# Optimization experiments

Hardware: AMD Instinct MI355X
Metric: run time of the kernel (lower is better)

Reference implementation:

```python
import jax, jax.numpy as jnp
import numpy as np

WINDOW = 8
HEADS = 16
HIDDEN = 256
EMBED = HIDDEN * WINDOW          # 2048
HEAD_DIM = EMBED // HEADS        # 128
BATCH = 8
SEQ = 4096                       # multiple of WINDOW
GROUP = SEQ // WINDOW            # 512


def _indices():
    # index_one[i*g + j] = j*w + i  (residue-class grouping permutation)
    i = np.arange(WINDOW)
    j = np.arange(GROUP)
    index_one = (j[None, :] * WINDOW + i[:, None]).reshape(-1)
    # index_two[i*w + k] = k*g + i  (inverse-style interleave permutation)
    index_two = (np.arange(WINDOW)[None, :] * GROUP + np.arange(GROUP)[:, None]).reshape(-1)
    return jnp.asarray(index_one), jnp.asarray(index_two)


def _attention(M, Wq, Wk, Wv, fc_w, fc_b):
    # M: [N, g, E] with E = heads*head_dim
    N, L, E = M.shape
    x = M.reshape(N, L, HEADS, HEAD_DIM)
    q = jnp.einsum('nlhd,ed->nlhe', x, Wq)
    k = jnp.einsum('nlhd,ed->nlhe', x, Wk)
    v = jnp.einsum('nlhd,ed->nlhe', x, Wv)
    energy = jnp.einsum('nqhd,nkhd->nhqk', q, k)
    attn = jax.nn.softmax(energy / jnp.sqrt(jnp.float32(EMBED)), axis=-1)
    out = jnp.einsum('nhqk,nkhd->nqhd', attn, v).reshape(N, L, E)
    return out @ fc_w.T + fc_b


def setup_inputs() -> dict:
    key = jax.random.key(0)
    ks = jax.random.split(key, 6)
    s = 0.02
    return {
        'M': jax.random.normal(ks[0], (BATCH, SEQ, HIDDEN), jnp.float32),
        'Wq': jax.random.normal(ks[1], (HEAD_DIM, HEAD_DIM), jnp.float32) * s,
        'Wk': jax.random.normal(ks[2], (HEAD_DIM, HEAD_DIM), jnp.float32) * s,
        'Wv': jax.random.normal(ks[3], (HEAD_DIM, HEAD_DIM), jnp.float32) * s,
        'fc_w': jax.random.normal(ks[4], (EMBED, EMBED), jnp.float32) * s,
        'fc_b': jax.random.normal(ks[5], (EMBED,), jnp.float32) * s,
        'device': 0,
    }


def reference(M, Wq, Wk, Wv, fc_w, fc_b, device):
    del device  # unused, mirrors torch signature
    index_one, index_two = _indices()
    N, S, H = M.shape
    w, g = WINDOW, GROUP
    for b in range(w):
        idx = (index_one - b) % S
        M = M[:, idx]                                             # gather permute
        # segmentation step 1: [N, w*g, H] -> [N, g, w*H]
        M = M.reshape(N, w, g, H).transpose(0, 2, 1, 3).reshape(N, g, w * H)
        M = _attention(M, Wq, Wk, Wv, fc_w, fc_b)
        # segmentation step 2: [N, g, w*H] -> [N, w*g, H]
        M = M.reshape(N, g, w, H).transpose(0, 2, 1, 3).reshape(N, w * g, H)
        # index_two rotated once per iteration after the first -> roll by -b
        M = M[:, jnp.roll(index_two, -b)]
    return M[:, :S]
```

## Files before the change

kernel.cpp:

```cpp
#include <hip/hip_runtime.h>
#include <stdint.h>

typedef unsigned short u16;
typedef unsigned int u32;
typedef __bf16 bf16x8 __attribute__((ext_vector_type(8)));
typedef float f32x4 __attribute__((ext_vector_type(4)));
typedef float f32x16 __attribute__((ext_vector_type(16)));
typedef u16 u16x4 __attribute__((ext_vector_type(4)));
typedef u16 u16x8 __attribute__((ext_vector_type(8)));

#define MFMA16(a, b, c) __builtin_amdgcn_mfma_f32_16x16x32_bf16(a, b, c, 0, 0, 0)
#define MFMA32(a, b, c) __builtin_amdgcn_mfma_f32_32x32x16_bf16(a, b, c, 0, 0, 0)

__device__ __forceinline__ u16 f2bf(float f) {
  u32 u = __builtin_bit_cast(u32, f);
  u += 0x7FFFu + ((u >> 16) & 1u);
  return (u16)(u >> 16);
}

__device__ __forceinline__ bf16x8 ld16(const u16* p) {
  return __builtin_bit_cast(bf16x8, *(const uint4*)p);
}

__device__ __forceinline__ void gl_lds(const u16* src, u16* lds) {
  __builtin_amdgcn_global_load_lds(
      (const __attribute__((address_space(1))) u32*)src,
      (__attribute__((address_space(3))) u32*)lds, 16, 0, 0);
}

__global__ __launch_bounds__(256) void convert_weights(
    const float* __restrict__ Wq, const float* __restrict__ Wk,
    const float* __restrict__ Wv, const float* __restrict__ fcw,
    u16* __restrict__ wq_b, u16* __restrict__ wk_b, u16* __restrict__ wv_b,
    u16* __restrict__ fcw_b) {
  int bx = blockIdx.x, tid = threadIdx.x;
  if (bx < 4096) {
    int i = (bx * 256 + tid) * 4;
    float4 f = *(const float4*)&fcw[i];
    u16x4 o = {f2bf(f.x), f2bf(f.y), f2bf(f.z), f2bf(f.w)};
    *(u16x4*)&fcw_b[i] = o;
  } else {
    int i = ((bx - 4096) * 256 + tid) * 4;
    const float sc = 0.022097086912079612f;
    float4 q = *(const float4*)&Wq[i];
    u16x4 oq = {f2bf(q.x * sc), f2bf(q.y * sc), f2bf(q.z * sc), f2bf(q.w * sc)};
    *(u16x4*)&wq_b[i] = oq;
    float4 k = *(const float4*)&Wk[i];
    u16x4 ok = {f2bf(k.x), f2bf(k.y), f2bf(k.z), f2bf(k.w)};
    *(u16x4*)&wk_b[i] = ok;
    float4 v = *(const float4*)&Wv[i];
    u16x4 ov = {f2bf(v.x), f2bf(v.y), f2bf(v.z), f2bf(v.w)};
    *(u16x4*)&wv_b[i] = ov;
  }
}

__global__ __launch_bounds__(768) void qkv_kernel(
    const float* __restrict__ srcF, const u16* __restrict__ srcB, int srcf32,
    const u16* __restrict__ wq, const u16* __restrict__ wk,
    const u16* __restrict__ wvw, u16* __restrict__ Q, u16* __restrict__ K,
    u16* __restrict__ Vt, int bsh) {
  __shared__ u16 X[64 * 264];
  int jt = blockIdx.x, i0 = blockIdx.y, n = blockIdx.z;
  int tid = threadIdx.x;
#pragma unroll
  for (int it = 0; it < 3; ++it) {
    int c = tid + it * 768;
    if (c < 2048) {
      int row = c >> 5, seg = c & 31;
      int pos = (8 * (jt * 64 + row) + i0 - bsh) & 4095;
      size_t base = ((size_t)n * 4096 + pos) * 256 + seg * 8;
      if (srcf32) {
        float4 f0 = *(const float4*)&srcF[base];
        float4 f1 = *(const float4*)&srcF[base + 4];
        u16x8 v = {f2bf(f0.x), f2bf(f0.y), f2bf(f0.z), f2bf(f0.w),
                   f2bf(f1.x), f2bf(f1.y), f2bf(f1.z), f2bf(f1.w)};
        *(u16x8*)&X[row * 264 + seg * 8] = v;
      } else {
        *(u16x8*)&X[row * 264 + seg * 8] = *(const u16x8*)&srcB[base];
      }
    }
  }
  __syncthreads();
  int wvid = tid >> 6, ln = tid & 63;
  int mat = wvid >> 2, hc = wvid & 3;
  int hh = hc >> 1, cb = (hc & 1) * 64;
  int h = i0 * 2 + hh, xc = hh * 128;
  const u16* W = (mat == 0) ? wq : (mat == 1) ? wk : wvw;
  int lr = ln & 15, lg = ln >> 4;
  f32x4 acc[4][4] = {};
#pragma unroll
  for (int kt = 0; kt < 4; ++kt) {
    bf16x8 a[4], b[4];
#pragma unroll
    for (int mt = 0; mt < 4; ++mt)
      a[mt] = ld16(&X[(mt * 16 + lr) * 264 + xc + kt * 32 + lg * 8]);
#pragma unroll
    for (int nc = 0; nc < 4; ++nc)
      b[nc] = ld16(&W[(cb + nc * 16 + lr) * 128 + kt * 32 + lg * 8]);
#pragma unroll
    for (int mt = 0; mt < 4; ++mt)
#pragma unroll
      for (int nc = 0; nc < 4; ++nc)
        acc[mt][nc] = MFMA16(a[mt], b[nc], acc[mt][nc]);
  }
  size_t nh = (size_t)(n * 16 + h);
  if (mat < 2) {
    u16* dst = (mat == 0 ? Q : K) + nh * 512 * 128;
#pragma unroll
    for (int mt = 0; mt < 4; ++mt)
#pragma unroll
      for (int nc = 0; nc < 4; ++nc) {
        int col = cb + nc * 16 + lr;
        int jb = jt * 64 + mt * 16 + lg * 4;
#pragma unroll
        for (int r = 0; r < 4; ++r)
          dst[(size_t)(jb + r) * 128 + col] = f2bf(acc[mt][nc][r]);
      }
  } else {
    u16* dst = Vt + nh * 128 * 512;
#pragma unroll
    for (int mt = 0; mt < 4; ++mt)
#pragma unroll
      for (int nc = 0; nc < 4; ++nc) {
        int col = cb + nc * 16 + lr;
        int jb = jt * 64 + mt * 16 + lg * 4;
        u16x4 pk = {f2bf(acc[mt][nc][0]), f2bf(acc[mt][nc][1]),
                    f2bf(acc[mt][nc][2]), f2bf(acc[mt][nc][3])};
        *(u16x4*)&dst[(size_t)col * 512 + jb] = pk;
      }
  }
}

__global__ __launch_bounds__(256, 2) void attn_kernel(
    const u16* __restrict__ Q, const u16* __restrict__ K,
    const u16* __restrict__ Vt, u16* __restrict__ O) {
  __shared__ u16 KL[2][64 * 128];
  __shared__ u16 VL[2][128 * 64];
  int flat = blockIdx.x;
  int xcd = flat & 7, idx = flat >> 3;
  int gl = idx & 15, qt = idx >> 4;
  int g = xcd | (gl << 3);
  int h = g & 15, n = g >> 4;
  int tid = threadIdx.x, wv = tid >> 6, ln = tid & 63;
  int l31 = ln & 31, hh = ln >> 5;
  size_t nh = (size_t)(n * 16 + h);
  int q0 = qt * 128 + wv * 32;
  const u16* Qb = Q + ((size_t)nh * 512 + q0) * 128;
  const u16* Kb = K + (size_t)nh * 512 * 128;
  const u16* Vb = Vt + (size_t)nh * 128 * 512;

  bf16x8 qf[8];
#pragma unroll
  for (int kt = 0; kt < 8; ++kt)
    qf[kt] = ld16(&Qb[l31 * 128 + kt * 16 + hh * 8]);

  int l16 = ln & 15, l8 = ln & 7;
  int rK[4], cK[4], rV[4], cV[4];
#pragma unroll
  for (int i = 0; i < 4; ++i) {
    int s = wv * 4 + i;
    rK[i] = 4 * s + (ln >> 4);
    cK[i] = (l16 ^ (rK[i] & 15)) * 8;
    rV[i] = 8 * s + (ln >> 3);
    cV[i] = (l8 ^ (rV[i] & 7)) * 8;
  }

#pragma unroll
  for (int i = 0; i < 4; ++i) {
    int s = wv * 4 + i;
    gl_lds(&Kb[(size_t)rK[i] * 128 + cK[i]], &KL[0][s * 512]);
    gl_lds(&Vb[(size_t)rV[i] * 512 + 0 * 64 + cV[i]], &VL[0][s * 512]);
  }
  __syncthreads();

  f32x16 o[4] = {};
  float m = -1e30f, l = 0.f;

  for (int kv = 0; kv < 8; ++kv) {
    int cur = kv & 1;
    if (kv < 7) {
      int nxt = cur ^ 1;
      const u16* kp = Kb + (size_t)(kv + 1) * 64 * 128;
#pragma unroll
      for (int i = 0; i < 4; ++i) {
        int s = wv * 4 + i;
        gl_lds(&kp[(size_t)rK[i] * 128 + cK[i]], &KL[nxt][s * 512]);
        gl_lds(&Vb[(size_t)rV[i] * 512 + (kv + 1) * 64 + cV[i]], &VL[nxt][s * 512]);
      }
    }
    f32x16 s[2] = {};
    __builtin_amdgcn_s_setprio(1);
#pragma unroll
    for (int kb = 0; kb < 2; ++kb)
#pragma unroll
      for (int kt = 0; kt < 8; ++kt) {
        int row = kb * 32 + l31;
        int slot = (2 * kt + hh) ^ (row & 15);
        bf16x8 a = ld16(&KL[cur][row * 128 + slot * 8]);
        s[kb] = MFMA32(a, qf[kt], s[kb]);
      }
    __builtin_amdgcn_s_setprio(0);
    float mx[8];
#pragma unroll
    for (int i = 0; i < 8; ++i)
      mx[i] = fmaxf(fmaxf(s[0][2 * i], s[0][2 * i + 1]),
                    fmaxf(s[1][2 * i], s[1][2 * i + 1]));
    float pm = fmaxf(fmaxf(fmaxf(mx[0], mx[1]), fmaxf(mx[2], mx[3])),
                     fmaxf(fmaxf(mx[4], mx[5]), fmaxf(mx[6], mx[7])));
    pm = fmaxf(pm, __shfl_xor(pm, 32));
    if (!__all(pm <= m + 8.f)) {
      float nm = fmaxf(m, pm);
      float al = __expf(m - nm);
      l *= al;
      m = nm;
#pragma unroll
      for (int r = 0; r < 16; ++r) {
        int qr = (r & 3) + 8 * (r >> 2) + 4 * hh;
        float av = __shfl(al, (ln & 32) | qr, 64);
        o[0][r] *= av; o[1][r] *= av; o[2][r] *= av; o[3][r] *= av;
      }
    }
#pragma unroll
    for (int kb = 0; kb < 2; ++kb)
#pragma unroll
      for (int r = 0; r < 16; ++r) s[kb][r] = __expf(s[kb][r] - m);
    float sm[8];
#pragma unroll
    for (int i = 0; i < 8; ++i)
      sm[i] = (s[0][2 * i] + s[0][2 * i + 1]) + (s[1][2 * i] + s[1][2 * i + 1]);
    float rs = ((sm[0] + sm[1]) + (sm[2] + sm[3])) +
               ((sm[4] + sm[5]) + (sm[6] + sm[7]));
    rs += __shfl_xor(rs, 32);
    l += rs;
    bf16x8 pa[4];
#pragma unroll
    for (int ks = 0; ks < 4; ++ks) {
      const int kb = ks >> 1, r0 = 8 * (ks & 1);
      u32 wA, wB, wC, wD;
      asm("v_cvt_pk_bf16_f32 %0, %1, %2" : "=v"(wA) : "v"(s[kb][r0 + 0]), "v"(s[kb][r0 + 1]));
      asm("v_cvt_pk_bf16_f32 %0, %1, %2" : "=v"(wB) : "v"(s[kb][r0 + 2]), "v"(s[kb][r0 + 3]));
      asm("v_cvt_pk_bf16_f32 %0, %1, %2" : "=v"(wC) : "v"(s[kb][r0 + 4]), "v"(s[kb][r0 + 5]));
      asm("v_cvt_pk_bf16_f32 %0, %1, %2" : "=v"(wD) : "v"(s[kb][r0 + 6]), "v"(s[kb][r0 + 7]));
      asm("v_permlane32_swap_b32 %0, %1" : "+v"(wA), "+v"(wC));
      asm("v_permlane32_swap_b32 %0, %1" : "+v"(wB), "+v"(wD));
      uint4 ww = {wA, wB, wC, wD};
      pa[ks] = __builtin_bit_cast(bf16x8, ww);
    }
    __builtin_amdgcn_s_setprio(1);
#pragma unroll
    for (int ks = 0; ks < 4; ++ks)
#pragma unroll
      for (int nb = 0; nb < 4; ++nb) {
        int row = nb * 32 + l31;
        int slot = (2 * ks + hh) ^ (row & 7);
        bf16x8 bv = ld16(&VL[cur][row * 64 + slot * 8]);
        o[nb] = MFMA32(pa[ks], bv, o[nb]);
      }
    __builtin_amdgcn_s_setprio(0);
    if (kv < 7) __syncthreads();
  }
  float inv = 1.f / l;
#pragma unroll
  for (int r = 0; r < 16; ++r) {
    int qr = (r & 3) + 8 * (r >> 2) + 4 * hh;
    float iv = __shfl(inv, (ln & 32) | qr, 64);
    int row = q0 + qr;
    u16* dst = O + ((size_t)n * 512 + row) * 2048 + h * 128;
    dst[0 * 32 + l31] = f2bf(o[0][r] * iv);
    dst[1 * 32 + l31] = f2bf(o[1][r] * iv);
    dst[2 * 32 + l31] = f2bf(o[2][r] * iv);
    dst[3 * 32 + l31] = f2bf(o[3][r] * iv);
  }
}

__global__ __launch_bounds__(256, 2) void fc_kernel(
    const u16* __restrict__ A, const u16* __restrict__ Bw,
    const float* __restrict__ bias, float* __restrict__ doutF,
    u16* __restrict__ doutB, int last, int bsh) {
  __shared__ u16 AL[2][128 * 64];
  __shared__ u16 BL[2][128 * 64];
  int bn = blockIdx.x, bm = blockIdx.y;
  int tid = threadIdx.x, wv = tid >> 6, ln = tid & 63;
  int lr = ln & 15, lg = ln >> 4;
  int R0 = bm * 128, C0 = bn * 128;
  int wr = (wv & 1) * 64, wc = (wv >> 1) * 64;
  const u16 *gAsrc[4], *gBsrc[4];
  int srow[4];
#pragma unroll
  for (int i = 0; i < 4; ++i) {
    int r = i * 32 + wv * 8 + (ln >> 3);
    int cs = ((ln & 7) ^ (r & 7)) * 8;
    gAsrc[i] = A + (size_t)(R0 + r) * 2048 + cs;
    gBsrc[i] = Bw + (size_t)(C0 + r) * 2048 + cs;
    srow[i] = i * 32 + wv * 8;
  }
  int aoff[4][2], boff[4][2];
#pragma unroll
  for (int i = 0; i < 4; ++i) {
    int ra = wr + i * 16 + lr, rb = wc + i * 16 + lr;
#pragma unroll
    for (int kk = 0; kk < 2; ++kk) {
      aoff[i][kk] = ra * 64 + (((kk * 4 + lg) ^ (ra & 7)) * 8);
      boff[i][kk] = rb * 64 + (((kk * 4 + lg) ^ (rb & 7)) * 8);
    }
  }
  f32x4 acc[4][4] = {};
#pragma unroll
  for (int i = 0; i < 4; ++i) {
    gl_lds(gAsrc[i], &AL[0][srow[i] * 64]);
    gl_lds(gBsrc[i], &BL[0][srow[i] * 64]);
  }
  for (int t = 0; t < 32; ++t) {
    int cur = t & 1, nx = cur ^ 1;
    if (t < 31) {
      int k0 = (t + 1) * 64;
#pragma unroll
      for (int i = 0; i < 4; ++i) {
        gl_lds(gAsrc[i] + k0, &AL[nx][srow[i] * 64]);
        gl_lds(gBsrc[i] + k0, &BL[nx][srow[i] * 64]);
      }
      asm volatile("s_waitcnt vmcnt(8)" ::: "memory");
    } else {
      asm volatile("s_waitcnt vmcnt(0)" ::: "memory");
    }
    __builtin_amdgcn_s_barrier();
#pragma unroll
    for (int kk = 0; kk < 2; ++kk) {
      bf16x8 a[4], b[4];
#pragma unroll
      for (int i = 0; i < 4; ++i) a[i] = ld16(&AL[cur][aoff[i][kk]]);
#pragma unroll
      for (int i = 0; i < 4; ++i) b[i] = ld16(&BL[cur][boff[i][kk]]);
      __builtin_amdgcn_s_setprio(1);
#pragma unroll
      for (int mt = 0; mt < 4; ++mt)
#pragma unroll
        for (int nc = 0; nc < 4; ++nc)
          acc[mt][nc] = MFMA16(a[mt], b[nc], acc[mt][nc]);
      __builtin_amdgcn_s_setprio(0);
    }
    if (t < 31) __builtin_amdgcn_s_barrier();
  }
#pragma unroll
  for (int nc = 0; nc < 4; ++nc) {
    int e = C0 + wc + nc * 16 + lr;
    float bv = bias[e];
    int i = e >> 8, cc = e & 255;
#pragma unroll
    for (int mt = 0; mt < 4; ++mt)
#pragma unroll
      for (int r = 0; r < 4; ++r) {
        int row = R0 + wr + mt * 16 + lg * 4 + r;
        int nn = row >> 9, j = row & 511;
        int pos = (8 * j + i - bsh) & 4095;
        size_t di = ((size_t)nn * 4096 + pos) * 256 + cc;
        float v = acc[mt][nc][r] + bv;
        if (last) doutF[di] = v;
        else doutB[di] = f2bf(v);
      }
  }
}

extern "C" void kernel_launch(void* const* d_in, const int* in_sizes, int n_in,
                              void* d_out, int out_size, void* d_ws, size_t ws_size,
                              hipStream_t stream) {
  const float* M = (const float*)d_in[0];
  const float* Wq = (const float*)d_in[1];
  const float* Wk = (const float*)d_in[2];
  const float* Wv = (const float*)d_in[3];
  const float* fcw = (const float*)d_in[4];
  const float* fcb = (const float*)d_in[5];
  float* out = (float*)d_out;
  char* ws = (char*)d_ws;
  u16* wq_b = (u16*)(ws + (0 << 10));
  u16* wk_b = (u16*)(ws + (32 << 10));
  u16* wv_b = (u16*)(ws + (64 << 10));
  u16* fcw_b = (u16*)(ws + (128 << 10));
  u16* Qb = (u16*)(ws + ((size_t)16 << 20));
  u16* Kb = (u16*)(ws + ((size_t)32 << 20));
  u16* Vtb = (u16*)(ws + ((size_t)48 << 20));
  u16* Ab = (u16*)(ws + ((size_t)64 << 20));
  u16* Sb = (u16*)(ws + ((size_t)96 << 20));

  convert_weights<<<4112, 256, 0, stream>>>(Wq, Wk, Wv, fcw, wq_b, wk_b, wv_b, fcw_b);
  for (int b = 0; b < 8; ++b) {
    qkv_kernel<<<dim3(8, 8, 8), 768, 0, stream>>>(M, Sb, (b == 0) ? 1 : 0,
                                                  wq_b, wk_b, wv_b, Qb, Kb, Vtb, b);
    attn_kernel<<<512, 256, 0, stream>>>(Qb, Kb, Vtb, Ab);
    fc_kernel<<<dim3(16, 32), 256, 0, stream>>>(Ab, fcw_b, fcb, out, Sb,
                                                (b == 7) ? 1 : 0, b);
  }
}
```

Measured before the change: 722.6 us.

## Enlarge FC GEMM tile to 128x256 with interleaved B-loads between MFMA phases

The FC GEMM now uses 512-thread blocks computing 128x256 output tiles (256 blocks instead of 512), so each A tile is reused across twice as many columns. The K-loop is split into four MFMA phases separated by barriers, and the next B tile's global-to-LDS loads are issued in halves between phases so memory traffic overlaps with compute. The intent is to cut global load traffic and hide load latency. In exchange it adds more barriers per iteration, needs more LDS per block, and 256 blocks may not fill all CUs as well as before.

```diff
diff --git a/kernel.cpp b/kernel.cpp
--- a/kernel.cpp
+++ b/kernel.cpp
@@ -273,26 +273,35 @@
   }
 }
 
-__global__ __launch_bounds__(256, 2) void fc_kernel(
+__global__ __launch_bounds__(512, 1) void fc_kernel(
     const u16* __restrict__ A, const u16* __restrict__ Bw,
     const float* __restrict__ bias, float* __restrict__ doutF,
     u16* __restrict__ doutB, int last, int bsh) {
   __shared__ u16 AL[2][128 * 64];
-  __shared__ u16 BL[2][128 * 64];
-  int bn = blockIdx.x, bm = blockIdx.y;
+  __shared__ u16 BL[2][256 * 64];
+  int blk = blockIdx.x;
+  int bm = blk >> 3, bn = blk & 7;
   int tid = threadIdx.x, wv = tid >> 6, ln = tid & 63;
   int lr = ln & 15, lg = ln >> 4;
-  int R0 = bm * 128, C0 = bn * 128;
-  int wr = (wv & 1) * 64, wc = (wv >> 1) * 64;
-  const u16 *gAsrc[4], *gBsrc[4];
-  int srow[4];
+  int R0 = bm * 128, C0 = bn * 256;
+  int wr = (wv >> 2) * 64, wc = (wv & 3) * 64;
+  const u16* gA[2];
+  int sA[2];
+  const u16* gB[4];
+  int sB[4];
+#pragma unroll
+  for (int i = 0; i < 2; ++i) {
+    int r = wv * 16 + i * 8 + (ln >> 3);
+    int cs = ((ln & 7) ^ (r & 7)) * 8;
+    gA[i] = A + (size_t)(R0 + r) * 2048 + cs;
+    sA[i] = (wv * 16 + i * 8) * 64;
+  }
 #pragma unroll
   for (int i = 0; i < 4; ++i) {
-    int r = i * 32 + wv * 8 + (ln >> 3);
+    int r = wv * 32 + i * 8 + (ln >> 3);
     int cs = ((ln & 7) ^ (r & 7)) * 8;
-    gAsrc[i] = A + (size_t)(R0 + r) * 2048 + cs;
-    gBsrc[i] = Bw + (size_t)(C0 + r) * 2048 + cs;
-    srow[i] = i * 32 + wv * 8;
+    gB[i] = Bw + (size_t)(C0 + r) * 2048 + cs;
+    sB[i] = (wv * 32 + i * 8) * 64;
   }
   int aoff[4][2], boff[4][2];
 #pragma unroll
@@ -306,40 +315,89 @@
   }
   f32x4 acc[4][4] = {};
 #pragma unroll
-  for (int i = 0; i < 4; ++i) {
-    gl_lds(gAsrc[i], &AL[0][srow[i] * 64]);
-    gl_lds(gBsrc[i], &BL[0][srow[i] * 64]);
-  }
+  for (int i = 0; i < 2; ++i) gl_lds(gA[i], &AL[0][sA[i]]);
+#pragma unroll
+  for (int i = 0; i < 4; ++i) gl_lds(gB[i], &BL[0][sB[i]]);
+
   for (int t = 0; t < 32; ++t) {
     int cur = t & 1, nx = cur ^ 1;
+    int k0 = (t + 1) * 64;
     if (t < 31) {
-      int k0 = (t + 1) * 64;
-#pragma unroll
-      for (int i = 0; i < 4; ++i) {
-        gl_lds(gAsrc[i] + k0, &AL[nx][srow[i] * 64]);
-        gl_lds(gBsrc[i] + k0, &BL[nx][srow[i] * 64]);
-      }
-      asm volatile("s_waitcnt vmcnt(8)" ::: "memory");
+      gl_lds(gA[0] + k0, &AL[nx][sA[0]]);
+      gl_lds(gA[1] + k0, &AL[nx][sA[1]]);
+      asm volatile("s_waitcnt vmcnt(2)" ::: "memory");
     } else {
       asm volatile("s_waitcnt vmcnt(0)" ::: "memory");
     }
     __builtin_amdgcn_s_barrier();
-#pragma unroll
-    for (int kk = 0; kk < 2; ++kk) {
-      bf16x8 a[4], b[4];
-#pragma unroll
-      for (int i = 0; i < 4; ++i) a[i] = ld16(&AL[cur][aoff[i][kk]]);
-#pragma unroll
-      for (int i = 0; i < 4; ++i) b[i] = ld16(&BL[cur][boff[i][kk]]);
+    bf16x8 b0 = ld16(&BL[cur][boff[0][0]]), b1 = ld16(&BL[cur][boff[1][0]]);
+    bf16x8 b2 = ld16(&BL[cur][boff[2][0]]), b3 = ld16(&BL[cur][boff[3][0]]);
+    {
+      bf16x8 a0 = ld16(&AL[cur][aoff[0][0]]), a1 = ld16(&AL[cur][aoff[1][0]]);
       __builtin_amdgcn_s_setprio(1);
-#pragma unroll
-      for (int mt = 0; mt < 4; ++mt)
-#pragma unroll
-        for (int nc = 0; nc < 4; ++nc)
-          acc[mt][nc] = MFMA16(a[mt], b[nc], acc[mt][nc]);
+      acc[0][0] = MFMA16(a0, b0, acc[0][0]);
+      acc[0][1] = MFMA16(a0, b1, acc[0][1]);
+      acc[0][2] = MFMA16(a0, b2, acc[0][2]);
+      acc[0][3] = MFMA16(a0, b3, acc[0][3]);
+      acc[1][0] = MFMA16(a1, b0, acc[1][0]);
+      acc[1][1] = MFMA16(a1, b1, acc[1][1]);
+      acc[1][2] = MFMA16(a1, b2, acc[1][2]);
+      acc[1][3] = MFMA16(a1, b3, acc[1][3]);
       __builtin_amdgcn_s_setprio(0);
     }
-    if (t < 31) __builtin_amdgcn_s_barrier();
+    __builtin_amdgcn_s_barrier();
+    if (t < 31) {
+      gl_lds(gB[0] + k0, &BL[nx][sB[0]]);
+      gl_lds(gB[1] + k0, &BL[nx][sB[1]]);
+    }
+    {
+      bf16x8 a2 = ld16(&AL[cur][aoff[2][0]]), a3 = ld16(&AL[cur][aoff[3][0]]);
+      __builtin_amdgcn_s_setprio(1);
+      acc[2][0] = MFMA16(a2, b0, acc[2][0]);
+      acc[2][1] = MFMA16(a2, b1, acc[2][1]);
+      acc[2][2] = MFMA16(a2, b2, acc[2][2]);
+      acc[2][3] = MFMA16(a2, b3, acc[2][3]);
+      acc[3][0] = MFMA16(a3, b0, acc[3][0]);
+      acc[3][1] = MFMA16(a3, b1, acc[3][1]);
+      acc[3][2] = MFMA16(a3, b2, acc[3][2]);
+      acc[3][3] = MFMA16(a3, b3, acc[3][3]);
+      __builtin_amdgcn_s_setprio(0);
+    }
+    __builtin_amdgcn_s_barrier();
+    if (t < 31) {
+      gl_lds(gB[2] + k0, &BL[nx][sB[2]]);
+      gl_lds(gB[3] + k0, &BL[nx][sB[3]]);
+    }
+    b0 = ld16(&BL[cur][boff[0][1]]); b1 = ld16(&BL[cur][boff[1][1]]);
+    b2 = ld16(&BL[cur][boff[2][1]]); b3 = ld16(&BL[cur][boff[3][1]]);
+    {
+      bf16x8 a0 = ld16(&AL[cur][aoff[0][1]]), a1 = ld16(&AL[cur][aoff[1][1]]);
+      __builtin_amdgcn_s_setprio(1);
+      acc[0][0] = MFMA16(a0, b0, acc[0][0]);
+      acc[0][1] = MFMA16(a0, b1, acc[0][1]);
+      acc[0][2] = MFMA16(a0, b2, acc[0][2]);
+      acc[0][3] = MFMA16(a0, b3, acc[0][3]);
+      acc[1][0] = MFMA16(a1, b0, acc[1][0]);
+      acc[1][1] = MFMA16(a1, b1, acc[1][1]);
+      acc[1][2] = MFMA16(a1, b2, acc[1][2]);
+      acc[1][3] = MFMA16(a1, b3, acc[1][3]);
+      __builtin_amdgcn_s_setprio(0);
+    }
+    __builtin_amdgcn_s_barrier();
+    {
+      bf16x8 a2 = ld16(&AL[cur][aoff[2][1]]), a3 = ld16(&AL[cur][aoff[3][1]]);
+      __builtin_amdgcn_s_setprio(1);
+      acc[2][0] = MFMA16(a2, b0, acc[2][0]);
+      acc[2][1] = MFMA16(a2, b1, acc[2][1]);
+      acc[2][2] = MFMA16(a2, b2, acc[2][2]);
+      acc[2][3] = MFMA16(a2, b3, acc[2][3]);
+      acc[3][0] = MFMA16(a3, b0, acc[3][0]);
+      acc[3][1] = MFMA16(a3, b1, acc[3][1]);
+      acc[3][2] = MFMA16(a3, b2, acc[3][2]);
+      acc[3][3] = MFMA16(a3, b3, acc[3][3]);
+      __builtin_amdgcn_s_setprio(0);
+    }
+    __builtin_amdgcn_s_barrier();
   }
 #pragma unroll
   for (int nc = 0; nc < 4; ++nc) {
@@ -387,7 +445,7 @@
     qkv_kernel<<<dim3(8, 8, 8), 768, 0, stream>>>(M, Sb, (b == 0) ? 1 : 0,
                                                   wq_b, wk_b, wv_b, Qb, Kb, Vtb, b);
     attn_kernel<<<512, 256, 0, stream>>>(Qb, Kb, Vtb, Ab);
-    fc_kernel<<<dim3(16, 32), 256, 0, stream>>>(Ab, fcw_b, fcb, out, Sb,
-                                                (b == 7) ? 1 : 0, b);
-  }
-}
+    fc_kernel<<<256, 512, 0, stream>>>(Ab, fcw_b, fcb, out, Sb,
+                                       (b == 7) ? 1 : 0, b);
+  }
+}
```

Measured after the change: 896.3 us. 24.0% more time.

## Software-pipeline QK^T one tile ahead with triple-buffered K in attention kernel

Applied to the files above, without the earlier changes.

Restructures the attention inner loop so the QK^T MFMAs for the next KV tile are issued before the softmax of the current tile, overlapping matrix work with the exp/reduction VALU work. K tiles move to a three-slot LDS ring loaded two tiles ahead, while V stays double-buffered, and the loop is fully unrolled. This costs extra LDS (one more 16KB K buffer) and more score registers held live at once, which may reduce occupancy or cause spills. The explicit priority hint around the QK^T MFMAs is dropped.

```diff
diff --git a/kernel.cpp b/kernel.cpp
--- a/kernel.cpp
+++ b/kernel.cpp
@@ -134,7 +134,7 @@
 __global__ __launch_bounds__(256, 2) void attn_kernel(
     const u16* __restrict__ Q, const u16* __restrict__ K,
     const u16* __restrict__ Vt, u16* __restrict__ O) {
-  __shared__ u16 KL[2][64 * 128];
+  __shared__ u16 KL[3][64 * 128];
   __shared__ u16 VL[2][128 * 64];
   int flat = blockIdx.x;
   int xcd = flat & 7, idx = flat >> 3;
@@ -165,46 +165,71 @@
     cV[i] = (l8 ^ (rV[i] & 7)) * 8;
   }
 
-#pragma unroll
-  for (int i = 0; i < 4; ++i) {
-    int s = wv * 4 + i;
-    gl_lds(&Kb[(size_t)rK[i] * 128 + cK[i]], &KL[0][s * 512]);
-    gl_lds(&Vb[(size_t)rV[i] * 512 + 0 * 64 + cV[i]], &VL[0][s * 512]);
-  }
+#define STAGE_K(buf, kv)                                                     \
+  {                                                                          \
+    const u16* kp_ = Kb + (size_t)(kv) * 64 * 128;                           \
+    _Pragma("unroll") for (int i_ = 0; i_ < 4; ++i_) {                       \
+      int s_ = wv * 4 + i_;                                                  \
+      gl_lds(&kp_[(size_t)rK[i_] * 128 + cK[i_]], &KL[buf][s_ * 512]);       \
+    }                                                                        \
+  }
+#define STAGE_V(buf, kv)                                                     \
+  {                                                                          \
+    _Pragma("unroll") for (int i_ = 0; i_ < 4; ++i_) {                       \
+      int s_ = wv * 4 + i_;                                                  \
+      gl_lds(&Vb[(size_t)rV[i_] * 512 + (kv)*64 + cV[i_]], &VL[buf][s_ * 512]); \
+    }                                                                        \
+  }
+
+  STAGE_K(0, 0);
+  STAGE_V(0, 0);
+  STAGE_K(1, 1);
   __syncthreads();
 
+  f32x16 ps[2][2];
   f32x16 o[4] = {};
   float m = -1e30f, l = 0.f;
 
-  for (int kv = 0; kv < 8; ++kv) {
-    int cur = kv & 1;
-    if (kv < 7) {
-      int nxt = cur ^ 1;
-      const u16* kp = Kb + (size_t)(kv + 1) * 64 * 128;
-#pragma unroll
-      for (int i = 0; i < 4; ++i) {
-        int s = wv * 4 + i;
-        gl_lds(&kp[(size_t)rK[i] * 128 + cK[i]], &KL[nxt][s * 512]);
-        gl_lds(&Vb[(size_t)rV[i] * 512 + (kv + 1) * 64 + cV[i]], &VL[nxt][s * 512]);
-      }
-    }
-    f32x16 s[2] = {};
-    __builtin_amdgcn_s_setprio(1);
-#pragma unroll
-    for (int kb = 0; kb < 2; ++kb)
+  {
+    f32x16 z = {};
+    ps[0][0] = z; ps[0][1] = z;
+#pragma unroll
+    for (int kt = 0; kt < 8; ++kt) {
+      int slot0 = (2 * kt + hh) ^ (l31 & 15);
+      bf16x8 a0 = ld16(&KL[0][l31 * 128 + slot0 * 8]);
+      ps[0][0] = MFMA32(a0, qf[kt], ps[0][0]);
+      int row1 = 32 + l31;
+      int slot1 = (2 * kt + hh) ^ (row1 & 15);
+      bf16x8 a1 = ld16(&KL[0][row1 * 128 + slot1 * 8]);
+      ps[0][1] = MFMA32(a1, qf[kt], ps[0][1]);
+    }
+  }
+
+#pragma unroll
+  for (int t = 0; t < 8; ++t) {
+    const int cur = t & 1, nxt = (t + 1) & 1;
+    if (t + 2 <= 7) STAGE_K((t + 2) % 3, t + 2);
+    if (t + 1 <= 7) STAGE_V(nxt, t + 1);
+    if (t + 1 <= 7) {
+      const int kb = (t + 1) % 3;
+      f32x16 z = {};
+      ps[nxt][0] = z; ps[nxt][1] = z;
 #pragma unroll
       for (int kt = 0; kt < 8; ++kt) {
-        int row = kb * 32 + l31;
-        int slot = (2 * kt + hh) ^ (row & 15);
-        bf16x8 a = ld16(&KL[cur][row * 128 + slot * 8]);
-        s[kb] = MFMA32(a, qf[kt], s[kb]);
-      }
-    __builtin_amdgcn_s_setprio(0);
+        int slot0 = (2 * kt + hh) ^ (l31 & 15);
+        bf16x8 a0 = ld16(&KL[kb][l31 * 128 + slot0 * 8]);
+        ps[nxt][0] = MFMA32(a0, qf[kt], ps[nxt][0]);
+        int row1 = 32 + l31;
+        int slot1 = (2 * kt + hh) ^ (row1 & 15);
+        bf16x8 a1 = ld16(&KL[kb][row1 * 128 + slot1 * 8]);
+        ps[nxt][1] = MFMA32(a1, qf[kt], ps[nxt][1]);
+      }
+    }
     float mx[8];
 #pragma unroll
     for (int i = 0; i < 8; ++i)
-      mx[i] = fmaxf(fmaxf(s[0][2 * i], s[0][2 * i + 1]),
-                    fmaxf(s[1][2 * i], s[1][2 * i + 1]));
+      mx[i] = fmaxf(fmaxf(ps[cur][0][2 * i], ps[cur][0][2 * i + 1]),
+                    fmaxf(ps[cur][1][2 * i], ps[cur][1][2 * i + 1]));
     float pm = fmaxf(fmaxf(fmaxf(mx[0], mx[1]), fmaxf(mx[2], mx[3])),
                      fmaxf(fmaxf(mx[4], mx[5]), fmaxf(mx[6], mx[7])));
     pm = fmaxf(pm, __shfl_xor(pm, 32));
@@ -221,13 +246,15 @@
       }
     }
 #pragma unroll
-    for (int kb = 0; kb < 2; ++kb)
-#pragma unroll
-      for (int r = 0; r < 16; ++r) s[kb][r] = __expf(s[kb][r] - m);
+    for (int kb2 = 0; kb2 < 2; ++kb2)
+#pragma unroll
+      for (int r = 0; r < 16; ++r)
+        ps[cur][kb2][r] = __expf(ps[cur][kb2][r] - m);
     float sm[8];
 #pragma unroll
     for (int i = 0; i < 8; ++i)
-      sm[i] = (s[0][2 * i] + s[0][2 * i + 1]) + (s[1][2 * i] + s[1][2 * i + 1]);
+      sm[i] = (ps[cur][0][2 * i] + ps[cur][0][2 * i + 1]) +
+              (ps[cur][1][2 * i] + ps[cur][1][2 * i + 1]);
     float rs = ((sm[0] + sm[1]) + (sm[2] + sm[3])) +
                ((sm[4] + sm[5]) + (sm[6] + sm[7]));
     rs += __shfl_xor(rs, 32);
@@ -235,12 +262,12 @@
     bf16x8 pa[4];
 #pragma unroll
     for (int ks = 0; ks < 4; ++ks) {
-      const int kb = ks >> 1, r0 = 8 * (ks & 1);
+      const int kb2 = ks >> 1, r0 = 8 * (ks & 1);
       u32 wA, wB, wC, wD;
-      asm("v_cvt_pk_bf16_f32 %0, %1, %2" : "=v"(wA) : "v"(s[kb][r0 + 0]), "v"(s[kb][r0 + 1]));
-      asm("v_cvt_pk_bf16_f32 %0, %1, %2" : "=v"(wB) : "v"(s[kb][r0 + 2]), "v"(s[kb][r0 + 3]));
-      asm("v_cvt_pk_bf16_f32 %0, %1, %2" : "=v"(wC) : "v"(s[kb][r0 + 4]), "v"(s[kb][r0 + 5]));
-      asm("v_cvt_pk_bf16_f32 %0, %1, %2" : "=v"(wD) : "v"(s[kb][r0 + 6]), "v"(s[kb][r0 + 7]));
+      asm("v_cvt_pk_bf16_f32 %0, %1, %2" : "=v"(wA) : "v"(ps[cur][kb2][r0 + 0]), "v"(ps[cur][kb2][r0 + 1]));
+      asm("v_cvt_pk_bf16_f32 %0, %1, %2" : "=v"(wB) : "v"(ps[cur][kb2][r0 + 2]), "v"(ps[cur][kb2][r0 + 3]));
+      asm("v_cvt_pk_bf16_f32 %0, %1, %2" : "=v"(wC) : "v"(ps[cur][kb2][r0 + 4]), "v"(ps[cur][kb2][r0 + 5]));
+      asm("v_cvt_pk_bf16_f32 %0, %1, %2" : "=v"(wD) : "v"(ps[cur][kb2][r0 + 6]), "v"(ps[cur][kb2][r0 + 7]));
       asm("v_permlane32_swap_b32 %0, %1" : "+v"(wA), "+v"(wC));
       asm("v_permlane32_swap_b32 %0, %1" : "+v"(wB), "+v"(wD));
       uint4 ww = {wA, wB, wC, wD};
@@ -257,8 +284,11 @@
         o[nb] = MFMA32(pa[ks], bv, o[nb]);
       }
     __builtin_amdgcn_s_setprio(0);
-    if (kv < 7) __syncthreads();
-  }
+    if (t < 7) __syncthreads();
+  }
+#undef STAGE_K
+#undef STAGE_V
+
   float inv = 1.f / l;
 #pragma unroll
   for (int r = 0; r < 16; ++r) {
```

New measurement: 721.2 us. Within noise of the previous version (-0.2%).
